# Optimization experiments

Measured on AMD Instinct MI355X. Metric: run time of the kernel, lower is better.

The kernel has to match this reference:

```python
import jax, jax.numpy as jnp
import numpy as np

B, N, D_MAX_LEN, D_LENGTH, D_MODEL, N_CLASS = 16, 1024, 512, 256, 128, 10
SAMPLE_K = 140  # factor(20) * ceil(ln(1024)) = 20*7; also n_top u (L_Q == L_K)


def setup_inputs() -> dict:
    key = jax.random.key(0)
    ks = jax.random.split(key, 10)
    s = 0.02
    return {
        "input_embedding": jax.random.normal(ks[0], (B, N, D_MAX_LEN), jnp.float32),
        "index_sample": jax.random.randint(ks[1], (N, SAMPLE_K), 0, N),
        # weights stored [in, out] (transpose of torch Linear.weight)
        "W_lin": jax.random.normal(ks[2], (D_MAX_LEN, D_LENGTH), jnp.float32) * s,
        "b_lin": jnp.zeros((D_LENGTH,), jnp.float32),
        "W_q": jax.random.normal(ks[3], (D_LENGTH, D_MODEL), jnp.float32) * s,
        "W_k": jax.random.normal(ks[4], (D_LENGTH, D_MODEL), jnp.float32) * s,
        "W_v": jax.random.normal(ks[5], (D_LENGTH, D_MODEL), jnp.float32) * s,
        "W_add": jax.random.normal(ks[6], (D_LENGTH, D_MODEL), jnp.float32) * s,
        "b_add": jnp.zeros((D_MODEL,), jnp.float32),
        "W_final": jax.random.normal(ks[7], (D_MODEL * N, N_CLASS), jnp.float32) * s,
        "b_final": jnp.zeros((N_CLASS,), jnp.float32),
    }


def reference(input_embedding, index_sample, W_lin, b_lin, W_q, W_k, W_v,
              W_add, b_add, W_final, b_final):
    # self.linear: [B, N, d_max_len] -> [B, N, d_length]
    x = input_embedding @ W_lin + b_lin
    b, n, _ = x.shape
    # single head (h=1): [B, 1, L, D]
    Q = (x @ W_q)[:, None]
    K = (x @ W_k)[:, None]
    V = (x @ W_v)[:, None]
    d = Q.shape[-1]
    L_K = n
    n_top = index_sample.shape[1]  # u == sample_k here

    # _prob_QK: gather sampled keys per query row, score against Q
    Kg = K[:, :, index_sample, :]                      # [B,1,L_Q,S,D]
    QK_sample = jnp.einsum('bhld,bhlsd->bhls', Q, Kg)  # [B,1,L_Q,S]
    M = QK_sample.max(-1) - QK_sample.sum(-1) / L_K    # sparsity measure
    _, M_top = jax.lax.top_k(M, n_top)                 # [B,1,u]

    Qr = jnp.take_along_axis(Q, M_top[..., None], axis=2)       # [B,1,u,D]
    scores = jnp.einsum('bhud,bhkd->bhuk', Qr, K) / np.sqrt(d)  # [B,1,u,L_K]

    # _get_initial_context (mask_flag=False): mean of V broadcast over L_Q
    ctx = jnp.broadcast_to(V.mean(axis=2, keepdims=True), V.shape)  # [B,1,L_Q,D]

    # _update_context: scatter softmax(scores) @ V into selected rows
    attn = jax.nn.softmax(scores, axis=-1)
    upd = jnp.einsum('bhuk,bhkd->bhud', attn, V)  # [B,1,u,D]
    bidx = jnp.arange(b)[:, None, None]
    hidx = jnp.arange(1)[None, :, None]
    ctx = ctx.at[bidx, hidx, M_top].set(upd)

    ctx = ctx[:, 0]                    # H=1 -> [B,N,D]
    out = ctx + (x @ W_add + b_add)    # residual add (dropout: eval mode)
    out = out.reshape(b, -1) @ W_final + b_final  # [B, n_class]
    return out
```

## Files before the change

### kernel.cpp

```cpp
#include <hip/hip_runtime.h>

typedef __attribute__((ext_vector_type(8))) short short8;
typedef __attribute__((ext_vector_type(4))) float f32x4;
typedef unsigned short u16;
typedef unsigned int u32;
typedef __attribute__((address_space(1))) const u32 gu32;
typedef __attribute__((address_space(3))) u32 lu32;

__device__ __forceinline__ u16 f2bf(float f){
  unsigned u = __float_as_uint(f);
  u += 0x7FFF + ((u >> 16) & 1);
  return (u16)(u >> 16);
}
__device__ __forceinline__ float bf2f(u16 h){ return __uint_as_float(((unsigned)h) << 16); }

#define BB   16
#define NN   1024
#define DML  512
#define DL   256
#define DM   128
#define NC   10
#define SK   140
#define KTOT (NN*DM)

__global__ void k_prep(const float* __restrict__ Wlin, const float* __restrict__ Wq,
                       const float* __restrict__ Wk, const float* __restrict__ Wv,
                       const float* __restrict__ Wadd,
                       u16* __restrict__ wlinT, u16* __restrict__ w4T,
                       const float* __restrict__ Wf, u16* __restrict__ wf2){
  int blk = blockIdx.x, t = threadIdx.x;
  if (blk < 512){
    int id = blk*256 + t;
    {
      int j = id >> 9;
      int k = id & 511;
      wlinT[id] = f2bf(Wlin[k*DL + j]);
    }
    {
      int j = id >> 8;
      int k = id & 255;
      const float* src = (j < 128) ? Wq : (j < 256) ? Wk : (j < 384) ? Wv : Wadd;
      int jj = j & 127;
      w4T[id] = f2bf(src[k*DM + jj]);
    }
  } else {
    int i4 = (blk-512)*256 + t;
    float4 v = ((const float4*)Wf)[i4];
    ushort4 o; o.x=f2bf(v.x); o.y=f2bf(v.y); o.z=f2bf(v.z); o.w=f2bf(v.w);
    ((ushort4*)wf2)[i4] = o;
  }
}

__device__ __forceinline__ void stage2(const u16* __restrict__ A, const u16* __restrict__ B,
                                       int K, int m0, int n0, int kb,
                                       u16* sA, u16* sB, int tid, int wave){
  #pragma unroll
  for (int i = 0; i < 4; ++i){
    int ci  = i*256 + tid;
    int row = ci >> 3;
    int kc  = (ci & 7) ^ (row & 7);
    __builtin_amdgcn_global_load_lds((gu32*)(A + (long)(m0+row)*K + kb + kc*8),
                                     (lu32*)(sA + (i*256 + wave*64)*8), 16, 0, 0);
    __builtin_amdgcn_global_load_lds((gu32*)(B + (long)(n0+row)*K + kb + kc*8),
                                     (lu32*)(sB + (i*256 + wave*64)*8), 16, 0, 0);
  }
}
__device__ __forceinline__ void compute64(const u16* sA, const u16* sB,
                                          int lane, int wrow, int wcol, f32x4 acc[4][4]){
  #pragma unroll
  for (int kk = 0; kk < 2; ++kk){
    short8 af[4], bfr[4];
    int cb = kk*4 + (lane >> 4);
    #pragma unroll
    for (int m_=0; m_<4; ++m_){
      int row = wrow + m_*16 + (lane & 15);
      af[m_] = *(const short8*)&sA[row*64 + ((cb ^ (row & 7)) << 3)];
    }
    #pragma unroll
    for (int n_=0; n_<4; ++n_){
      int row = wcol + n_*16 + (lane & 15);
      bfr[n_] = *(const short8*)&sB[row*64 + ((cb ^ (row & 7)) << 3)];
    }
    #pragma unroll
    for (int m_=0; m_<4; ++m_)
      #pragma unroll
      for (int n_=0; n_<4; ++n_)
        acc[m_][n_] = __builtin_amdgcn_mfma_f32_16x16x32_bf16(af[m_], bfr[n_], acc[m_][n_], 0, 0, 0);
  }
}
__device__ __forceinline__ void gemm_core_db(const u16* __restrict__ A, const u16* __restrict__ B,
                                             int K, int m0, int n0,
                                             u16* sA0, u16* sB0, u16* sA1, u16* sB1,
                                             f32x4 acc[4][4]){
  const int tid  = threadIdx.x;
  const int lane = tid & 63;
  const int wave = tid >> 6;
  const int wrow = (wave >> 1) * 64;
  const int wcol = (wave & 1) * 64;
  u16 *cA = sA0, *cB = sB0, *nA = sA1, *nB = sB1;
  stage2(A, B, K, m0, n0, 0, cA, cB, tid, wave);
  __syncthreads();
  int nt = K >> 6;
  for (int t = 0; t < nt-1; ++t){
    stage2(A, B, K, m0, n0, (t+1)*64, nA, nB, tid, wave);
    compute64(cA, cB, lane, wrow, wcol, acc);
    __syncthreads();
    u16* x;
    x = cA; cA = nA; nA = x;
    x = cB; cB = nB; nB = x;
  }
  compute64(cA, cB, lane, wrow, wcol, acc);
}

__global__ __launch_bounds__(256) void k_gemm_x(const float* __restrict__ A, const u16* __restrict__ B,
                                                const float* __restrict__ bias, u16* __restrict__ out){
  __shared__ u16 smem[12288];
  u16* sA = smem;
  u16* sB = smem + 4096;
  const int tid  = threadIdx.x;
  const int lane = tid & 63;
  const int wave = tid >> 6;
  const int wrow = (wave >> 1) * 32;
  const int wcol = (wave & 1) * 64;
  int m0 = blockIdx.x*64, n0 = blockIdx.y*128;
  f32x4 acc[2][4];
  f32x4 z = {0.f,0.f,0.f,0.f};
  #pragma unroll
  for (int m_=0;m_<2;++m_) for (int n_=0;n_<4;++n_) acc[m_][n_] = z;

  f32x4 ra[4];
  short8 rb[4];
  const int arow = tid >> 2, aq = tid & 3;

  {
    const float* src = A + (long)(m0+arow)*DML + aq*16;
    ra[0] = ((const f32x4*)src)[0]; ra[1] = ((const f32x4*)src)[1];
    ra[2] = ((const f32x4*)src)[2]; ra[3] = ((const f32x4*)src)[3];
    #pragma unroll
    for (int i=0;i<4;++i){
      int ci = i*256 + tid, row = ci>>3, kc = ci&7;
      rb[i] = *(const short8*)(B + (long)(n0+row)*DML + kc*8);
    }
  }
  {
    short8 o0, o1;
    #pragma unroll
    for (int j=0;j<4;++j){ o0[j]=(short)f2bf(ra[0][j]); o0[4+j]=(short)f2bf(ra[1][j]);
                           o1[j]=(short)f2bf(ra[2][j]); o1[4+j]=(short)f2bf(ra[3][j]); }
    int kc0 = aq*2, kc1 = aq*2+1;
    *(short8*)&sA[arow*64 + ((kc0 ^ (arow&7))<<3)] = o0;
    *(short8*)&sA[arow*64 + ((kc1 ^ (arow&7))<<3)] = o1;
    #pragma unroll
    for (int i=0;i<4;++i){
      int ci = i*256 + tid, row = ci>>3, kc = ci&7;
      *(short8*)&sB[row*64 + ((kc ^ (row&7))<<3)] = rb[i];
    }
  }
  __syncthreads();

  for (int tt = 0; tt < 8; ++tt){
    if (tt < 7){
      int kb = (tt+1)*64;
      const float* src = A + (long)(m0+arow)*DML + kb + aq*16;
      ra[0] = ((const f32x4*)src)[0]; ra[1] = ((const f32x4*)src)[1];
      ra[2] = ((const f32x4*)src)[2]; ra[3] = ((const f32x4*)src)[3];
      #pragma unroll
      for (int i=0;i<4;++i){
        int ci = i*256 + tid, row = ci>>3, kc = ci&7;
        rb[i] = *(const short8*)(B + (long)(n0+row)*DML + kb + kc*8);
      }
    }
    #pragma unroll
    for (int kk = 0; kk < 2; ++kk){
      short8 af[2], bfr[4];
      int cb = kk*4 + (lane >> 4);
      #pragma unroll
      for (int m_=0; m_<2; ++m_){
        int row = wrow + m_*16 + (lane & 15);
        af[m_] = *(const short8*)&sA[row*64 + ((cb ^ (row & 7)) << 3)];
      }
      #pragma unroll
      for (int n_=0; n_<4; ++n_){
        int row = wcol + n_*16 + (lane & 15);
        bfr[n_] = *(const short8*)&sB[row*64 + ((cb ^ (row & 7)) << 3)];
      }
      #pragma unroll
      for (int m_=0; m_<2; ++m_)
        #pragma unroll
        for (int n_=0; n_<4; ++n_)
          acc[m_][n_] = __builtin_amdgcn_mfma_f32_16x16x32_bf16(af[m_], bfr[n_], acc[m_][n_], 0, 0, 0);
    }
    __syncthreads();
    if (tt < 7){
      short8 o0, o1;
      #pragma unroll
      for (int j=0;j<4;++j){ o0[j]=(short)f2bf(ra[0][j]); o0[4+j]=(short)f2bf(ra[1][j]);
                             o1[j]=(short)f2bf(ra[2][j]); o1[4+j]=(short)f2bf(ra[3][j]); }
      int kc0 = aq*2, kc1 = aq*2+1;
      *(short8*)&sA[arow*64 + ((kc0 ^ (arow&7))<<3)] = o0;
      *(short8*)&sA[arow*64 + ((kc1 ^ (arow&7))<<3)] = o1;
      #pragma unroll
      for (int i=0;i<4;++i){
        int ci = i*256 + tid, row = ci>>3, kc = ci&7;
        *(short8*)&sB[row*64 + ((kc ^ (row&7))<<3)] = rb[i];
      }
      __syncthreads();
    }
  }

  u16* sC = sB;
  #pragma unroll
  for (int m_=0;m_<2;++m_)
    #pragma unroll
    for (int n_=0;n_<4;++n_)
      #pragma unroll
      for (int rr=0;rr<4;++rr){
        int row = wrow + m_*16 + (lane>>4)*4 + rr;
        int col = wcol + n_*16 + (lane & 15);
        sC[row*128 + col] = f2bf(acc[m_][n_][rr] + bias[n0 + col]);
      }
  __syncthreads();
  #pragma unroll
  for (int i = 0; i < 4; ++i){
    int ci = i*256 + tid;
    int row = ci >> 4, c = ci & 15;
    *(short8*)(out + (long)(m0+row)*DL + n0 + c*8) = *(const short8*)&sC[row*128 + c*8];
  }
}

__global__ __launch_bounds__(256) void k_gemm_qkva(const u16* __restrict__ A, const u16* __restrict__ B,
                                                   const float* __restrict__ badd,
                                                   u16* __restrict__ oq, u16* __restrict__ ok,
                                                   u16* __restrict__ ov, u16* __restrict__ oa){
  __shared__ u16 smem[32768];
  f32x4 acc[4][4];
  f32x4 z = {0.f,0.f,0.f,0.f};
  #pragma unroll
  for (int m_=0;m_<4;++m_) for (int n_=0;n_<4;++n_) acc[m_][n_] = z;
  int m0 = blockIdx.x*128;
  int tn = blockIdx.y;
  gemm_core_db(A, B, DL, m0, tn*128, smem, smem+8192, smem+16384, smem+24576, acc);
  int tid = threadIdx.x, lane = tid & 63, wave = tid >> 6;
  int wrow = (wave>>1)*64, wcol = (wave&1)*64;
  u16* dst = (tn==0) ? oq : (tn==1) ? ok : (tn==2) ? ov : oa;

  u16* sC = smem;
  #pragma unroll
  for (int m_=0;m_<4;++m_)
    #pragma unroll
    for (int n_=0;n_<4;++n_)
      #pragma unroll
      for (int r=0;r<4;++r){
        int row = wrow + m_*16 + (lane>>4)*4 + r;
        int col = wcol + n_*16 + (lane & 15);
        float v = acc[m_][n_][r];
        if (tn == 3) v += badd[col];
        sC[row*128 + col] = f2bf(v);
      }
  __syncthreads();
  u16* db = dst + (long)m0*DM;
  #pragma unroll
  for (int i = 0; i < 8; ++i){
    int ci = i*256 + tid;
    int row = ci >> 4, c = ci & 15;
    *(short8*)(db + (long)row*DM + c*8) = *(const short8*)&sC[row*128 + c*8];
  }
}

__global__ __launch_bounds__(256) void k_gemm_s(const u16* __restrict__ Q, const u16* __restrict__ Km,
                                                u16* __restrict__ S){
  __shared__ u16 smem[32768];
  u16* sA0 = smem;
  u16* sB0 = smem + 8192;
  u16* sA1 = smem + 16384;
  u16* sB1 = smem + 24576;
  const int tid = threadIdx.x, lane = tid & 63, wave = tid >> 6;
  const int wrow = (wave>>1)*64, wcol = (wave&1)*64;
  f32x4 acc[4][4];
  f32x4 z = {0.f,0.f,0.f,0.f};
  #pragma unroll
  for (int m_=0;m_<4;++m_) for (int n_=0;n_<4;++n_) acc[m_][n_] = z;
  int b = blockIdx.z, m0 = blockIdx.x*128, n0 = blockIdx.y*128;
  const u16* A = Q  + (long)b*NN*DM;
  const u16* B = Km + (long)b*NN*DM;

  stage2(A, B, DM, m0, n0, 0, sA0, sB0, tid, wave);
  __syncthreads();
  stage2(A, B, DM, m0, n0, 64, sA1, sB1, tid, wave);
  compute64(sA0, sB0, lane, wrow, wcol, acc);
  __syncthreads();
  compute64(sA1, sB1, lane, wrow, wcol, acc);

  u16* sS = smem;
  #pragma unroll
  for (int m_=0;m_<4;++m_)
    #pragma unroll
    for (int n_=0;n_<4;++n_)
      #pragma unroll
      for (int r=0;r<4;++r){
        int row = wrow + m_*16 + (lane>>4)*4 + r;
        int col = wcol + n_*16 + (lane & 15);
        sS[row*128 + col] = f2bf(acc[m_][n_][r]);
      }
  __syncthreads();

  u16* Sb = S + (long)b*NN*NN + (long)m0*NN + n0;
  #pragma unroll
  for (int i = 0; i < 8; ++i){
    int ci = i*256 + tid;
    int row = ci >> 4, c = ci & 15;
    *(short8*)(Sb + (long)row*NN + c*8) = *(const short8*)&sS[row*128 + c*8];
  }
}

__global__ void k_mscore(const u16* __restrict__ S, const int* __restrict__ idx, float* __restrict__ M){
  int g    = blockIdx.x*4 + (threadIdx.x >> 6);
  int lane = threadIdx.x & 63;
  int b = g >> 10, l = g & 1023;
  const u16* Srow = S + (long)b*NN*NN + (long)l*NN;
  const int* ir = idx + l*SK;
  float mx = -1e30f, sm = 0.f;
  for (int s = lane; s < SK; s += 64){
    float v = bf2f(Srow[ir[s]]);
    mx = fmaxf(mx, v); sm += v;
  }
  #pragma unroll
  for (int o=32;o;o>>=1){ mx = fmaxf(mx, __shfl_xor(mx,o)); sm += __shfl_xor(sm,o); }
  if (lane == 0) M[g] = mx - sm * (1.0f/1024.0f);
}

__global__ __launch_bounds__(256) void k_rankvm(const float* __restrict__ M, int* __restrict__ partial,
                                                const u16* __restrict__ V, float* __restrict__ vmean){
  __shared__ float sC[64];
  __shared__ float red[16][128];
  int blk = blockIdx.x, t = threadIdx.x;
  if (blk < 256){
    int jc = blk & 15, b = blk >> 4;
    const float* Mb = M + b*NN;
    if (t < 64) sC[t] = Mb[jc*64 + t];
    __syncthreads();
    int j0 = jc*64;
    float mi[4];
    int cnt[4] = {0,0,0,0};
    #pragma unroll
    for (int r=0;r<4;++r) mi[r] = Mb[t + r*256];
    for (int j = 0; j < 64; ++j){
      float mj = sC[j];
      int jg = j0 + j;
      #pragma unroll
      for (int r=0;r<4;++r){
        int i = t + r*256;
        cnt[r] += (mj > mi[r]) || (mj == mi[r] && jg < i);
      }
    }
    int* pb = partial + (b*16 + jc)*NN;
    #pragma unroll
    for (int r=0;r<4;++r) pb[t + r*256] = cnt[r];
  } else {
    int b = blk - 256;
    int d8 = t & 15, seg = t >> 4;
    const u16* Vb = V + (long)b*KTOT + seg*64*DM + d8*8;
    float acc[8] = {0,0,0,0,0,0,0,0};
    for (int l = 0; l < 64; ++l){
      short8 v = *(const short8*)(Vb + l*DM);
      #pragma unroll
      for (int j=0;j<8;++j) acc[j] += bf2f((u16)v[j]);
    }
    #pragma unroll
    for (int j=0;j<8;++j) red[seg][d8*8+j] = acc[j];
    __syncthreads();
    if (t < 128){
      float s = 0.f;
      #pragma unroll
      for (int g=0;g<16;++g) s += red[g][t];
      vmean[b*DM + t] = s * (1.0f/1024.0f);
    }
  }
}

__global__ __launch_bounds__(1024) void k_sel(const int* __restrict__ partial, int* __restrict__ mtop,
                                              int* __restrict__ selmap){
  int b = blockIdx.x, i = threadIdx.x;
  int cnt = 0;
  #pragma unroll
  for (int jc = 0; jc < 16; ++jc) cnt += partial[(b*16 + jc)*NN + i];
  selmap[b*NN + i] = (cnt < SK) ? cnt : -1;
  if (cnt < SK) mtop[b*SK + cnt] = i;
}

__global__ __launch_bounds__(256) void k_attn(const u16* __restrict__ S, const u16* __restrict__ V,
                                              const int* __restrict__ mtop, float* __restrict__ upd){
  __shared__ float sE[4][1024];
  __shared__ float redM[4][4];
  __shared__ float redS[4][4];
  __shared__ float sP[4][4][128];
  int b = blockIdx.y, u0 = blockIdx.x*4, t = threadIdx.x;
  int lane = t & 63, wave = t >> 6;
  const float inv = 0.08838834764831845f;

  int rows[4];
  #pragma unroll
  for (int r=0;r<4;++r) rows[r] = mtop[b*SK + u0 + r];

  float sv[4][4];
  float pm[4];
  const u16* Sb = S + (long)b*NN*NN;
  #pragma unroll
  for (int r=0;r<4;++r){
    ushort4 raw = ((const ushort4*)(Sb + (long)rows[r]*NN))[t];
    sv[r][0] = bf2f(raw.x)*inv; sv[r][1] = bf2f(raw.y)*inv;
    sv[r][2] = bf2f(raw.z)*inv; sv[r][3] = bf2f(raw.w)*inv;
    pm[r] = fmaxf(fmaxf(sv[r][0],sv[r][1]), fmaxf(sv[r][2],sv[r][3]));
  }
  #pragma unroll
  for (int o=32;o;o>>=1)
    #pragma unroll
    for (int r=0;r<4;++r) pm[r] = fmaxf(pm[r], __shfl_xor(pm[r],o));
  if (lane == 0){
    #pragma unroll
    for (int r=0;r<4;++r) redM[wave][r] = pm[r];
  }
  __syncthreads();
  float mx[4], ps[4];
  #pragma unroll
  for (int r=0;r<4;++r)
    mx[r] = fmaxf(fmaxf(redM[0][r],redM[1][r]), fmaxf(redM[2][r],redM[3][r]));
  #pragma unroll
  for (int r=0;r<4;++r){
    float s = 0.f;
    #pragma unroll
    for (int j=0;j<4;++j){
      float e = __expf(sv[r][j] - mx[r]);
      sE[r][t*4+j] = e;
      s += e;
    }
    ps[r] = s;
  }
  #pragma unroll
  for (int o=32;o;o>>=1)
    #pragma unroll
    for (int r=0;r<4;++r) ps[r] += __shfl_xor(ps[r],o);
  if (lane == 0){
    #pragma unroll
    for (int r=0;r<4;++r) redS[wave][r] = ps[r];
  }
  __syncthreads();
  float rZ[4];
  #pragma unroll
  for (int r=0;r<4;++r)
    rZ[r] = 1.0f / (redS[0][r]+redS[1][r]+redS[2][r]+redS[3][r]);

  int dg = t & 15;
  int kg = t >> 4;
  const u16* Vb = V + (long)b*KTOT + dg*8;
  float acc[4][8];
  #pragma unroll
  for (int r=0;r<4;++r)
    #pragma unroll
    for (int j=0;j<8;++j) acc[r][j] = 0.f;

  for (int k = kg; k < NN; k += 16){
    short8 v = *(const short8*)(Vb + (long)k*DM);
    float vf[8];
    #pragma unroll
    for (int j=0;j<8;++j) vf[j] = bf2f((u16)v[j]);
    #pragma unroll
    for (int r=0;r<4;++r){
      float e = sE[r][k];
      #pragma unroll
      for (int j=0;j<8;++j) acc[r][j] += e * vf[j];
    }
  }

  #pragma unroll
  for (int o=16;o<64;o<<=1)
    #pragma unroll
    for (int r=0;r<4;++r)
      #pragma unroll
      for (int j=0;j<8;++j) acc[r][j] += __shfl_xor(acc[r][j], o);

  if ((t & 63) < 16){
    #pragma unroll
    for (int r=0;r<4;++r)
      #pragma unroll
      for (int j=0;j<8;++j) sP[wave][r][dg*8+j] = acc[r][j];
  }
  __syncthreads();
  if (t < 128){
    #pragma unroll
    for (int r=0;r<4;++r){
      float s = sP[0][r][t] + sP[1][r][t] + sP[2][r][t] + sP[3][r][t];
      upd[((long)b*SK + u0 + r)*DM + t] = s * rZ[r];
    }
  }
}

__global__ __launch_bounds__(256) void k_final(const float* __restrict__ upd, const float* __restrict__ vmean,
                                               const int* __restrict__ selmap,
                                               const u16* __restrict__ Aad,
                                               const u16* __restrict__ wf2, float* __restrict__ part){
  int b = blockIdx.x, ch = blockIdx.y, t = threadIdx.x;
  long base = (long)b * KTOT;
  int k0 = ch * 4096;
  float acc[NC] = {0.f};
  for (int k = k0 + t; k < k0 + 4096; k += 256){
    int l = k >> 7, d = k & 127;
    int sel = selmap[b*NN + l];
    float c = (sel >= 0) ? upd[((long)b*SK + sel)*DM + d] : vmean[b*DM + d];
    float v = c + bf2f(Aad[base + k]);
    const u32* w32 = (const u32*)(wf2 + (long)k*NC);
    #pragma unroll
    for (int cc = 0; cc < 5; ++cc){
      u32 w = w32[cc];
      acc[2*cc]   += v * bf2f((u16)(w & 0xFFFF));
      acc[2*cc+1] += v * bf2f((u16)(w >> 16));
    }
  }
  __shared__ float lred[40];
  int lane = t & 63, wave = t >> 6;
  #pragma unroll
  for (int c = 0; c < NC; ++c){
    float v = acc[c];
    #pragma unroll
    for (int o=32;o;o>>=1) v += __shfl_xor(v,o);
    if (lane == 0) lred[wave*NC + c] = v;
  }
  __syncthreads();
  if (t < NC) part[(b*32 + ch)*NC + t] = lred[t] + lred[NC+t] + lred[2*NC+t] + lred[3*NC+t];
}

__global__ void k_out(const float* __restrict__ part, const float* __restrict__ bfin, float* __restrict__ out){
  int t = threadIdx.x;
  if (t < BB*NC){
    int b = t / NC, c = t % NC;
    float s = bfin[c];
    #pragma unroll
    for (int ch = 0; ch < 32; ++ch) s += part[(b*32 + ch)*NC + c];
    out[t] = s;
  }
}

extern "C" void kernel_launch(void* const* d_in, const int* in_sizes, int n_in,
                              void* d_out, int out_size, void* d_ws, size_t ws_size,
                              hipStream_t stream){
  const float* emb  = (const float*)d_in[0];
  const int*   idxs = (const int*)  d_in[1];
  const float* Wlin = (const float*)d_in[2];
  const float* blin = (const float*)d_in[3];
  const float* Wq   = (const float*)d_in[4];
  const float* Wk   = (const float*)d_in[5];
  const float* Wv   = (const float*)d_in[6];
  const float* Wadd = (const float*)d_in[7];
  const float* badd = (const float*)d_in[8];
  const float* Wfin = (const float*)d_in[9];
  const float* bfin = (const float*)d_in[10];
  float* out = (float*)d_out;

  char* p = (char*)d_ws;
  auto alloc = [&](size_t bytes)->char*{ char* r = p; p += (bytes + 255) & ~(size_t)255; return r; };
  u16*   wlinT  = (u16*)  alloc((size_t)DL*DML*2);
  u16*   w4T    = (u16*)  alloc((size_t)4*DM*DL*2);
  u16*   x_bf   = (u16*)  alloc((size_t)BB*NN*DL*2);
  u16*   q_bf   = (u16*)  alloc((size_t)BB*NN*DM*2);
  u16*   k_bf   = (u16*)  alloc((size_t)BB*NN*DM*2);
  u16*   v_bf   = (u16*)  alloc((size_t)BB*NN*DM*2);
  u16*   a_bf   = (u16*)  alloc((size_t)BB*NN*DM*2);
  u16*   s_bf   = (u16*)  alloc((size_t)BB*NN*NN*2);
  float* m_f    = (float*)alloc((size_t)BB*NN*4);
  int*   rankp  = (int*)  alloc((size_t)BB*16*NN*4);
  int*   mtop   = (int*)  alloc((size_t)BB*SK*4);
  int*   selmap = (int*)  alloc((size_t)BB*NN*4);
  float* vmean  = (float*)alloc((size_t)BB*DM*4);
  float* upd    = (float*)alloc((size_t)BB*SK*DM*4);
  u16*   wf2    = (u16*)  alloc((size_t)KTOT*NC*2);
  float* part   = (float*)alloc((size_t)BB*32*NC*4);

  k_prep<<<dim3(1792), dim3(256), 0, stream>>>(Wlin, Wq, Wk, Wv, Wadd, wlinT, w4T, Wfin, wf2);
  k_gemm_x<<<dim3(256, 2), dim3(256), 0, stream>>>(emb, wlinT, blin, x_bf);
  k_gemm_qkva<<<dim3(128, 4), dim3(256), 0, stream>>>(x_bf, w4T, badd, q_bf, k_bf, v_bf, a_bf);
  k_gemm_s<<<dim3(8, 8, 16), dim3(256), 0, stream>>>(q_bf, k_bf, s_bf);
  k_mscore<<<dim3(BB*NN/4), dim3(256), 0, stream>>>(s_bf, idxs, m_f);
  k_rankvm<<<dim3(272), dim3(256), 0, stream>>>(m_f, rankp, v_bf, vmean);
  k_sel<<<dim3(BB), dim3(1024), 0, stream>>>(rankp, mtop, selmap);
  k_attn<<<dim3(SK/4, BB), dim3(256), 0, stream>>>(s_bf, v_bf, mtop, upd);
  k_final<<<dim3(BB, 32), dim3(256), 0, stream>>>(upd, vmean, selmap, a_bf, wf2, part);
  k_out<<<dim3(1), dim3(256), 0, stream>>>(part, bfin, out);
}
```

Before: 113.2 us.

## Reorder grids batch-fastest for L2/XCD locality and halve gemm_s LDS

Three kernels (score GEMM, mscore, attention) now launch with the batch index as the fastest-varying grid dimension, so consecutively dispatched blocks cover different batches. On MI355X, blocks are distributed round-robin across XCDs, so this is meant to change which S rows and Q/K tiles end up in each XCD's L2. The score GEMM also drops its double-buffered shared memory (64KB to 32KB) and instead reuses one buffer with extra barriers. That should raise occupancy but serializes loading and computing of the two K chunks.

```diff
diff --git a/kernel.cpp b/kernel.cpp
--- a/kernel.cpp
+++ b/kernel.cpp
@@ -269,27 +269,27 @@
 
 __global__ __launch_bounds__(256) void k_gemm_s(const u16* __restrict__ Q, const u16* __restrict__ Km,
                                                 u16* __restrict__ S){
-  __shared__ u16 smem[32768];
-  u16* sA0 = smem;
-  u16* sB0 = smem + 8192;
-  u16* sA1 = smem + 16384;
-  u16* sB1 = smem + 24576;
+  __shared__ u16 smem[16384];
+  u16* sA = smem;
+  u16* sB = smem + 8192;
   const int tid = threadIdx.x, lane = tid & 63, wave = tid >> 6;
   const int wrow = (wave>>1)*64, wcol = (wave&1)*64;
   f32x4 acc[4][4];
   f32x4 z = {0.f,0.f,0.f,0.f};
   #pragma unroll
   for (int m_=0;m_<4;++m_) for (int n_=0;n_<4;++n_) acc[m_][n_] = z;
-  int b = blockIdx.z, m0 = blockIdx.x*128, n0 = blockIdx.y*128;
+  int b = blockIdx.x, n0 = blockIdx.y*128, m0 = blockIdx.z*128;
   const u16* A = Q  + (long)b*NN*DM;
   const u16* B = Km + (long)b*NN*DM;
 
-  stage2(A, B, DM, m0, n0, 0, sA0, sB0, tid, wave);
-  __syncthreads();
-  stage2(A, B, DM, m0, n0, 64, sA1, sB1, tid, wave);
-  compute64(sA0, sB0, lane, wrow, wcol, acc);
-  __syncthreads();
-  compute64(sA1, sB1, lane, wrow, wcol, acc);
+  stage2(A, B, DM, m0, n0, 0, sA, sB, tid, wave);
+  __syncthreads();
+  compute64(sA, sB, lane, wrow, wcol, acc);
+  __syncthreads();
+  stage2(A, B, DM, m0, n0, 64, sA, sB, tid, wave);
+  __syncthreads();
+  compute64(sA, sB, lane, wrow, wcol, acc);
+  __syncthreads();
 
   u16* sS = smem;
   #pragma unroll
@@ -314,9 +314,9 @@
 }
 
 __global__ void k_mscore(const u16* __restrict__ S, const int* __restrict__ idx, float* __restrict__ M){
-  int g    = blockIdx.x*4 + (threadIdx.x >> 6);
+  int b = blockIdx.x;
+  int l = blockIdx.y*4 + (threadIdx.x >> 6);
   int lane = threadIdx.x & 63;
-  int b = g >> 10, l = g & 1023;
   const u16* Srow = S + (long)b*NN*NN + (long)l*NN;
   const int* ir = idx + l*SK;
   float mx = -1e30f, sm = 0.f;
@@ -326,7 +326,7 @@
   }
   #pragma unroll
   for (int o=32;o;o>>=1){ mx = fmaxf(mx, __shfl_xor(mx,o)); sm += __shfl_xor(sm,o); }
-  if (lane == 0) M[g] = mx - sm * (1.0f/1024.0f);
+  if (lane == 0) M[b*NN + l] = mx - sm * (1.0f/1024.0f);
 }
 
 __global__ __launch_bounds__(256) void k_rankvm(const float* __restrict__ M, int* __restrict__ partial,
@@ -394,7 +394,7 @@
   __shared__ float redM[4][4];
   __shared__ float redS[4][4];
   __shared__ float sP[4][4][128];
-  int b = blockIdx.y, u0 = blockIdx.x*4, t = threadIdx.x;
+  int b = blockIdx.x, u0 = blockIdx.y*4, t = threadIdx.x;
   int lane = t & 63, wave = t >> 6;
   const float inv = 0.08838834764831845f;
 
@@ -578,11 +578,11 @@
   k_prep<<<dim3(1792), dim3(256), 0, stream>>>(Wlin, Wq, Wk, Wv, Wadd, wlinT, w4T, Wfin, wf2);
   k_gemm_x<<<dim3(256, 2), dim3(256), 0, stream>>>(emb, wlinT, blin, x_bf);
   k_gemm_qkva<<<dim3(128, 4), dim3(256), 0, stream>>>(x_bf, w4T, badd, q_bf, k_bf, v_bf, a_bf);
-  k_gemm_s<<<dim3(8, 8, 16), dim3(256), 0, stream>>>(q_bf, k_bf, s_bf);
-  k_mscore<<<dim3(BB*NN/4), dim3(256), 0, stream>>>(s_bf, idxs, m_f);
+  k_gemm_s<<<dim3(16, 8, 8), dim3(256), 0, stream>>>(q_bf, k_bf, s_bf);
+  k_mscore<<<dim3(BB, NN/4), dim3(256), 0, stream>>>(s_bf, idxs, m_f);
   k_rankvm<<<dim3(272), dim3(256), 0, stream>>>(m_f, rankp, v_bf, vmean);
   k_sel<<<dim3(BB), dim3(1024), 0, stream>>>(rankp, mtop, selmap);
-  k_attn<<<dim3(SK/4, BB), dim3(256), 0, stream>>>(s_bf, v_bf, mtop, upd);
+  k_attn<<<dim3(BB, SK/4), dim3(256), 0, stream>>>(s_bf, v_bf, mtop, upd);
   k_final<<<dim3(BB, 32), dim3(256), 0, stream>>>(upd, vmean, selmap, a_bf, wf2, part);
   k_out<<<dim3(1), dim3(256), 0, stream>>>(part, bfin, out);
 }
```

Result: faster. 104.6 us (-7.6%).
